# Performance work log

Measured on AMD Instinct MI355X. Metric: run time of the kernel, lower is better.

## Reference

```python
import jax, jax.numpy as jnp
import numpy as np

MODEL_DIM = 128
N_FRAMES = 128
N_SAMPLES = 32768
N_TABLES = 8
TABLE_SIZE = 512
BATCH = 8
N_FREQS = 16


def _mlp(x, w1, b1, w2, b2, w3, b3):
    # LinearOutputStack(channels, 3, ...): Linear -> lrelu -> Linear -> lrelu -> Linear
    h = jax.nn.leaky_relu(x @ w1 + b1, 0.2)
    h = jax.nn.leaky_relu(h @ w2 + b2, 0.2)
    return h @ w3 + b3


def _pos_encoded(t, n_freqs=N_FREQS):
    # (t, 1 + 2*n_freqs) = (t, 33): raw position plus sin/cos at geometric freqs
    pos = jnp.linspace(-1.0, 1.0, t, dtype=jnp.float32)
    scales = (2.0 ** jnp.arange(n_freqs, dtype=jnp.float32)) * jnp.pi
    ang = pos[:, None] * scales[None, :]
    return jnp.concatenate([pos[:, None], jnp.sin(ang), jnp.cos(ang)], axis=-1)


def _interp_linear(env, out_size):
    # torch F.interpolate(mode='linear', align_corners=False) from (B, F) to (B, out_size)
    f = env.shape[-1]
    coord = (jnp.arange(out_size, dtype=jnp.float32) + 0.5) * (f / out_size) - 0.5
    i0 = jnp.floor(coord)
    frac = (coord - i0).astype(env.dtype)
    i0c = jnp.clip(i0, 0, f - 1).astype(jnp.int32)
    i1c = jnp.clip(i0 + 1, 0, f - 1).astype(jnp.int32)
    return env[:, i0c] * (1.0 - frac) + env[:, i1c] * frac


def setup_inputs() -> dict:
    key = jax.random.key(0)
    ks = jax.random.split(key, 16)
    wi = 0.02  # weight_init from Experiment
    d = MODEL_DIM

    def lin(k, i, o):
        return jax.random.normal(k, (i, o), jnp.float32) * wi

    inp = {
        "x": jax.random.normal(ks[0], (BATCH, d), jnp.float32),
        "wavetables": jax.random.uniform(ks[1], (N_TABLES, TABLE_SIZE), jnp.float32, -1.0, 1.0),
    }
    specs = {"tc": (d, N_TABLES), "env": (d, N_FRAMES), "pos": (33, d), "sk": (d, TABLE_SIZE)}
    i = 2
    for name, (cin, cout) in specs.items():
        k1, k2, k3 = jax.random.split(ks[i], 3)
        inp[f"{name}_w1"] = lin(k1, cin, d)
        inp[f"{name}_b1"] = jnp.zeros((d,), jnp.float32)
        inp[f"{name}_w2"] = lin(k2, d, d)
        inp[f"{name}_b2"] = jnp.zeros((d,), jnp.float32)
        inp[f"{name}_w3"] = lin(k3, d, cout)
        inp[f"{name}_b3"] = jnp.zeros((cout,), jnp.float32)
        i += 1
    return inp


def reference(x, wavetables,
              tc_w1, tc_b1, tc_w2, tc_b2, tc_w3, tc_b3,
              env_w1, env_b1, env_w2, env_b2, env_w3, env_b3,
              pos_w1, pos_b1, pos_w2, pos_b2, pos_w3, pos_b3,
              sk_w1, sk_b1, sk_w2, sk_b2, sk_w3, sk_b3):
    # table choice: softmax then hard max (straight value * gathered table)
    c = jax.nn.softmax(_mlp(x, tc_w1, tc_b1, tc_w2, tc_b2, tc_w3, tc_b3), axis=-1)
    values = jnp.max(c, axis=-1)          # (B,)
    indices = jnp.argmax(c, axis=-1)      # (B,)

    mx = jnp.max(wavetables, axis=-1, keepdims=True)
    wt = wavetables / (mx + 1e-8)
    sel = wt[indices]                     # (B, TABLE_SIZE)

    env = jnp.abs(_mlp(x, env_w1, env_b1, env_w2, env_b2, env_w3, env_b3))  # (B, N_FRAMES)
    env = _interp_linear(env, N_SAMPLES)  # (B, N_SAMPLES)

    # pos encoding is identical across batch; embed once then broadcast (same math)
    pe = _pos_encoded(N_SAMPLES)          # (T, 33)
    pos = _mlp(pe, pos_w1, pos_b1, pos_w2, pos_b2, pos_w3, pos_b3)  # (T, D)
    pos = pos[None, :, :] + x[:, None, :]  # (B, T, D)

    sk = jax.nn.softmax(_mlp(pos, sk_w1, sk_b1, sk_w2, sk_b2, sk_w3, sk_b3), axis=-1)  # (B, T, K)

    # selected_tables (B,1,K) @ kernel^T (B,K,T) -> (B,1,T)
    sampled = jnp.einsum('bk,btk->bt', sel, sk)
    sampled = sampled * env * values[:, None]
    return sampled[:, None, :]
```

## Files before the change

### kernel.cpp

```cpp
#include <hip/hip_runtime.h>
#include <math.h>

#define D 128
#define B 8
#define T_SAMP 32768
#define K 512
#define NT 8
#define NFRM 128

#define WS_C1   0
#define WS_ENV8 1024
#define WS_SEL  2048
#define WS_VAL  6144
#define WS_B3P  6160
#define WSBF_BYTE 32768
#define OP1 0
#define OP2 9216
#define OP3 26624
#define OS1 44032
#define OS2 61440
#define OS3 78848
#define WTOT 148480
#define WS_NEED (WSBF_BYTE + WTOT*2)

typedef __attribute__((ext_vector_type(8))) short short8;
typedef __attribute__((ext_vector_type(4))) float f32x4;

#define LOG2E 1.4426950408889634f

__device__ __forceinline__ float lrelu(float v){ return fmaxf(v, 0.2f*v); }

__device__ __forceinline__ unsigned cvtpk(float lo, float hi){
    unsigned r;
    asm("v_cvt_pk_bf16_f32 %0, %1, %2" : "=v"(r) : "v"(lo), "v"(hi));
    return r;
}
__device__ __forceinline__ unsigned short bfr(float f){
    unsigned u = __builtin_bit_cast(unsigned, f); u += 0x7fffu + ((u>>16)&1u);
    return (unsigned short)(u>>16);
}
__device__ __forceinline__ float bf2f(short s){
    unsigned u = ((unsigned)(unsigned short)s) << 16;
    return __builtin_bit_cast(float, u);
}
__device__ __forceinline__ float exp2fast(float x){
#if __has_builtin(__builtin_amdgcn_exp2f)
    return __builtin_amdgcn_exp2f(x);
#else
    return __expf(x*0.6931471805599453f);
#endif
}
__device__ __forceinline__ float sin_rev(float fr){
#if __has_builtin(__builtin_amdgcn_sinf)
    return __builtin_amdgcn_sinf(fr);
#else
    return __sinf(fr*6.283185307179586f);
#endif
}
__device__ __forceinline__ float cos_rev(float fr){
#if __has_builtin(__builtin_amdgcn_cosf)
    return __builtin_amdgcn_cosf(fr);
#else
    return __cosf(fr*6.283185307179586f);
#endif
}
__device__ __forceinline__ float pe_val(float pf, int j){
    if (j == 0) return pf;
    if (j > 32) return 0.f;
    const bool is_sin = (j <= 16);
    int e = is_sin ? (j + 125) : (j + 109);
    float sc = __builtin_bit_cast(float, ((unsigned)e) << 23);
    float u = pf * sc;
    float fr = u - floorf(u);
    return is_sin ? sin_rev(fr) : cos_rev(fr);
}

#define VMCNT0 asm volatile("s_waitcnt vmcnt(0)" ::: "memory")

__device__ void layer128(const float* __restrict__ in, const float* __restrict__ w,
                         const float* __restrict__ bias, float* __restrict__ outp,
                         int tid, int mode)
{
    int n = tid & 127, bg = tid >> 7;
    const float* i0 = in + (bg*4+0)*D;
    const float* i1 = in + (bg*4+1)*D;
    const float* i2 = in + (bg*4+2)*D;
    const float* i3 = in + (bg*4+3)*D;
    float bb = bias[n];
    float a0=bb,a1=bb,a2=bb,a3=bb;
    for (int j=0;j<D;j++){
        float wv = w[j*D+n];
        a0 = fmaf(i0[j], wv, a0);
        a1 = fmaf(i1[j], wv, a1);
        a2 = fmaf(i2[j], wv, a2);
        a3 = fmaf(i3[j], wv, a3);
    }
    if (mode==0){ a0=lrelu(a0);a1=lrelu(a1);a2=lrelu(a2);a3=lrelu(a3); }
    else if (mode==1){ a0=fabsf(a0);a1=fabsf(a1);a2=fabsf(a2);a3=fabsf(a3); }
    outp[(bg*4+0)*D+n]=a0;
    outp[(bg*4+1)*D+n]=a1;
    outp[(bg*4+2)*D+n]=a2;
    outp[(bg*4+3)*D+n]=a3;
}

__global__ __launch_bounds__(256) void setup_kernel(
    const float* __restrict__ x, const float* __restrict__ wt,
    const float* __restrict__ tc_w1, const float* __restrict__ tc_b1,
    const float* __restrict__ tc_w2, const float* __restrict__ tc_b2,
    const float* __restrict__ tc_w3, const float* __restrict__ tc_b3,
    const float* __restrict__ env_w1, const float* __restrict__ env_b1,
    const float* __restrict__ env_w2, const float* __restrict__ env_b2,
    const float* __restrict__ env_w3, const float* __restrict__ env_b3,
    const float* __restrict__ sk_w1, const float* __restrict__ sk_b1,
    const float* __restrict__ pos_w1, const float* __restrict__ pos_w2,
    const float* __restrict__ pos_w3, const float* __restrict__ sk_w2,
    const float* __restrict__ sk_w3, const float* __restrict__ sk_b3,
    float* __restrict__ ws)
{
    __shared__ float xl[B*D], buf1[B*D], buf2[B*D];
    __shared__ float lgts[B*NT], pmax[NT*8], mxr[NT];
    __shared__ int idxl[B];
    int tid = threadIdx.x;

    if (blockIdx.x != 0){
        int idx = (blockIdx.x - 1)*256 + tid;
        if (idx >= WTOT) return;
        unsigned short* wb = (unsigned short*)((char*)ws + WSBF_BYTE);
        float v;
        if (idx < OP2){
            int n = idx/72, k = idx%72;
            v = (k < 33) ? pos_w1[k*D + n] : 0.f;
        } else if (idx < OS3){
            int r = idx - OP2; int wsel = r/17408; int i = r%17408;
            int n = i/136, k = i%136;
            const float* W = wsel==0?pos_w2: wsel==1?pos_w3: wsel==2? sk_w1 : sk_w2;
            v = (k < 128) ? W[k*D + n] : 0.f;
        } else {
            int i = idx - OS3; int n = i/136, k = i%136;
            v = (k < 128) ? sk_w3[k*K + n] : 0.f;
        }
        wb[idx] = bfr(v);
        return;
    }

    for (int i=tid;i<B*D;i+=256) xl[i]=x[i];
    for (int i=tid;i<K;i+=256) ws[WS_B3P+i] = sk_b3[i]*LOG2E;
    __syncthreads();
    layer128(xl, tc_w1, tc_b1, buf1, tid, 0);
    __syncthreads();
    layer128(buf1, tc_w2, tc_b2, buf2, tid, 0);
    __syncthreads();
    if (tid < 64){
        int b = tid>>3, n = tid&7;
        float a = tc_b3[n];
        for (int j=0;j<D;j++) a = fmaf(buf2[b*D+j], tc_w3[j*NT+n], a);
        lgts[b*NT+n] = a;
    } else if (tid < 128){
        int r = (tid-64)>>3, p = tid&7;
        float m = -1e30f;
        for (int k=p*64;k<p*64+64;k++) m = fmaxf(m, wt[r*K+k]);
        pmax[r*8+p] = m;
    }
    __syncthreads();
    if (tid < 8){
        int b = tid; float m = -1e30f; int idx = 0;
        for (int n=0;n<NT;n++){ float v = lgts[b*NT+n]; if (v > m){ m=v; idx=n; } }
        float S = 0.f;
        for (int n=0;n<NT;n++) S += expf(lgts[b*NT+n]-m);
        ws[WS_VAL+b] = 1.0f/S;
        idxl[b] = idx;
    } else if (tid < 16){
        int r = tid-8; float m = -1e30f;
        for (int p=0;p<8;p++) m = fmaxf(m, pmax[r*8+p]);
        mxr[r] = m;
    }
    __syncthreads();
    for (int o=tid;o<B*K;o+=256){
        int b = o>>9, k = o&(K-1);
        int id = idxl[b];
        ws[WS_SEL+o] = wt[id*K+k] / (mxr[id] + 1e-8f);
    }
    layer128(xl, env_w1, env_b1, buf1, tid, 0);
    __syncthreads();
    layer128(buf1, env_w2, env_b2, buf2, tid, 0);
    __syncthreads();
    layer128(buf2, env_w3, env_b3, ws+WS_ENV8, tid, 1);
    layer128(xl, sk_w1, sk_b1, ws+WS_C1, tid, 2);
}

template<int NKT, int KSTR, bool ACT>
__device__ __forceinline__ void layerF(const short8* aw,
                                       const unsigned char* inb, unsigned char* outb,
                                       const float* biasp, int wv, int lg, int lc)
{
    const f32x4 z = {0.f,0.f,0.f,0.f};
    f32x4 bb = z;
    if (biasp) bb = *(const f32x4*)(biasp + 16*wv + 4*lg);
    #pragma unroll
    for (int rt=0;rt<2;rt++){
        f32x4 d = z;
        #pragma unroll
        for (int kt=0;kt<NKT;kt++){
            short8 bf = *(const short8*)(inb + ((16*rt+lc)*KSTR + 32*kt + 8*lg)*2);
            d = __builtin_amdgcn_mfma_f32_16x16x32_bf16(aw[kt], bf, d, 0,0,0);
        }
        float o0 = d[0]+bb[0], o1 = d[1]+bb[1], o2 = d[2]+bb[2], o3 = d[3]+bb[3];
        if (ACT){ o0=lrelu(o0); o1=lrelu(o1); o2=lrelu(o2); o3=lrelu(o3); }
        uint2 u; u.x = cvtpk(o0,o1); u.y = cvtpk(o2,o3);
        *(uint2*)(outb + ((16*rt+lc)*136 + 16*wv + 4*lg)*2) = u;
    }
}

__global__ __launch_bounds__(512, 4) void synth6(
    const float* __restrict__ pos_b1, const float* __restrict__ pos_b2,
    const float* __restrict__ pos_b3, const float* __restrict__ sk_b2,
    const float* __restrict__ ws, float* __restrict__ out)
{
    __shared__ __align__(16) unsigned char lds[34816];
    unsigned char* abA = lds;
    unsigned char* abB = lds + 9216;
    unsigned char* PEb = abB;

    const int tid = threadIdx.x;
    const int wv = tid >> 6, lane = tid & 63, lg = lane >> 4, lc = lane & 15;
    const int t0 = blockIdx.x * 32;
    const unsigned short* wg16 = (const unsigned short*)((const char*)ws + WSBF_BYTE);
    const f32x4 z = {0.f,0.f,0.f,0.f};

    short8 aw1[2];
    #pragma unroll
    for (int kt=0;kt<2;kt++)
        aw1[kt] = *(const short8*)(wg16 + OP1 + (16*wv+lc)*72 + 32*kt + 8*lg);
    for (int i = tid; i < 1152; i += 512){
        int r = i/36, j0 = (i - r*36)*2;
        float pf = (float)(-1.0 + 2.0*(double)(t0+r)/32767.0);
        float v0 = pe_val(pf, j0);
        float v1 = pe_val(pf, j0+1);
        *(unsigned*)(PEb + (r*72 + j0)*2) = cvtpk(v0, v1);
    }
    __syncthreads();

    short8 awn[4];
    #pragma unroll
    for (int kt=0;kt<4;kt++)
        awn[kt] = *(const short8*)(wg16 + OP2 + (16*wv+lc)*136 + 32*kt + 8*lg);
    layerF<2,72,true>(aw1, PEb, abA, pos_b1, wv, lg, lc);
    __syncthreads();

    {
        short8 awp[4];
        #pragma unroll
        for (int kt=0;kt<4;kt++)
            awp[kt] = *(const short8*)(wg16 + OP3 + (16*wv+lc)*136 + 32*kt + 8*lg);
        layerF<4,136,true>(awn, abA, abB, pos_b2, wv, lg, lc);
        #pragma unroll
        for (int kt=0;kt<4;kt++) awn[kt] = awp[kt];
    }
    __syncthreads();

    {
        short8 awp[4];
        #pragma unroll
        for (int kt=0;kt<4;kt++)
            awp[kt] = *(const short8*)(wg16 + OS1 + (16*wv+lc)*136 + 32*kt + 8*lg);
        layerF<4,136,false>(awn, abB, abA, pos_b3, wv, lg, lc);
        #pragma unroll
        for (int kt=0;kt<4;kt++) awn[kt] = awp[kt];
    }
    __syncthreads();

    layerF<4,136,false>(awn, abA, abB, nullptr, wv, lg, lc);
    __syncthreads();

    {
        const unsigned char* src = (const unsigned char*)(wg16 + OS2);
        for (int c = wv; c < 34; c += 8)
            if (c < 9 || c >= 18)
                __builtin_amdgcn_global_load_lds(
                    (const __attribute__((address_space(1))) unsigned int*)(src + (c<<10) + lane*16),
                    (__attribute__((address_space(3))) unsigned int*)(lds + (c<<10)), 16, 0, 0);
    }

    short8 hf[2][4];
    {
        const int b = lc & 7;
        const float* c1g = ws + WS_C1 + b*128;
        #pragma unroll
        for (int rtl=0;rtl<2;rtl++){
            int tl = 4*wv + 2*rtl + (lc>>3);
            #pragma unroll
            for (int kt=0;kt<4;kt++){
                short8 a1v = *(const short8*)(abB + (tl*136 + 32*kt + 8*lg)*2);
                const float* cp = c1g + 32*kt + 8*lg;
                f32x4 c0 = *(const f32x4*)cp;
                f32x4 c1v = *(const f32x4*)(cp+4);
                float h[8];
                #pragma unroll
                for (int e=0;e<4;e++){
                    h[e]   = lrelu(bf2f(a1v[e])   + c0[e]);
                    h[4+e] = lrelu(bf2f(a1v[4+e]) + c1v[e]);
                }
                uint4 t4; t4.x=cvtpk(h[0],h[1]); t4.y=cvtpk(h[2],h[3]);
                t4.z=cvtpk(h[4],h[5]); t4.w=cvtpk(h[6],h[7]);
                hf[rtl][kt] = __builtin_bit_cast(short8, t4);
            }
        }
    }
    __syncthreads();

    {
        const unsigned char* src = (const unsigned char*)(wg16 + OS2);
        for (int c = 9 + wv; c < 18; c += 8)
            __builtin_amdgcn_global_load_lds(
                (const __attribute__((address_space(1))) unsigned int*)(src + (c<<10) + lane*16),
                (__attribute__((address_space(3))) unsigned int*)(lds + (c<<10)), 16, 0, 0);
    }
    VMCNT0; __syncthreads();

    short8 h2B[2][4];
    {
        const int sA = (2*(lg&1))*16 + lc;
        const int sB = sA + 16;
        const bool hi = (lg>>1) != 0;
        __builtin_amdgcn_s_setprio(1);
        #pragma unroll
        for (int kt2=0; kt2<4; kt2++){
            unsigned dpk[2][2][2];
            #pragma unroll
            for (int p=0;p<2;p++){
                int n2t = 2*kt2+p;
                short8 aw[4];
                #pragma unroll
                for (int kt=0;kt<4;kt++)
                    aw[kt] = *(const short8*)(lds + ((16*n2t+lc)*136 + 32*kt + 8*lg)*2);
                f32x4 b2 = *(const f32x4*)(sk_b2 + 16*n2t + 4*lg);
                #pragma unroll
                for (int rtl=0;rtl<2;rtl++){
                    f32x4 d = z;
                    #pragma unroll
                    for (int kt=0;kt<4;kt++)
                        d = __builtin_amdgcn_mfma_f32_16x16x32_bf16(aw[kt], hf[rtl][kt], d, 0,0,0);
                    float o0=lrelu(d[0]+b2[0]), o1=lrelu(d[1]+b2[1]);
                    float o2=lrelu(d[2]+b2[2]), o3=lrelu(d[3]+b2[3]);
                    dpk[p][rtl][0] = cvtpk(o0,o1);
                    dpk[p][rtl][1] = cvtpk(o2,o3);
                }
            }
            #pragma unroll
            for (int rtl=0;rtl<2;rtl++){
                unsigned a0 = (unsigned)__shfl((int)dpk[0][rtl][0], sA, 64);
                unsigned b0 = (unsigned)__shfl((int)dpk[1][rtl][0], sA, 64);
                unsigned a1 = (unsigned)__shfl((int)dpk[0][rtl][1], sA, 64);
                unsigned b1 = (unsigned)__shfl((int)dpk[1][rtl][1], sA, 64);
                unsigned a2 = (unsigned)__shfl((int)dpk[0][rtl][0], sB, 64);
                unsigned b2u= (unsigned)__shfl((int)dpk[1][rtl][0], sB, 64);
                unsigned a3 = (unsigned)__shfl((int)dpk[0][rtl][1], sB, 64);
                unsigned b3u= (unsigned)__shfl((int)dpk[1][rtl][1], sB, 64);
                uint4 uu;
                uu.x = hi ? b0 : a0;  uu.y = hi ? b1 : a1;
                uu.z = hi ? b2u : a2; uu.w = hi ? b3u : a3;
                h2B[rtl][kt2] = __builtin_bit_cast(short8, uu);
            }
        }
        __builtin_amdgcn_s_setprio(0);
    }
    __syncthreads();

    float SSa[2][4], WWa[2][4];
    #pragma unroll
    for (int r=0;r<2;r++)
        #pragma unroll
        for (int q=0;q<4;q++){ SSa[r][q]=0.f; WWa[r][q]=0.f; }

    auto stage = [&](int elemoff, unsigned char* dst, int nchunks){
        const unsigned char* src = (const unsigned char*)(wg16 + elemoff);
        for (int c = wv; c < nchunks; c += 8)
            __builtin_amdgcn_global_load_lds(
                (const __attribute__((address_space(1))) unsigned int*)(src + (c<<10) + lane*16),
                (__attribute__((address_space(3))) unsigned int*)(dst + (c<<10)), 16, 0, 0);
    };

    stage(OS3, lds, 17); VMCNT0; __syncthreads();
    const float* selg = ws + WS_SEL + (lc & 7)*512;
    const float* b3g  = ws + WS_B3P;
    for (int c=0;c<8;c++){
        const unsigned char* slot = lds + (c&1)*17408;
        if (c < 7) stage(OS3 + (c+1)*8704, lds + ((c+1)&1)*17408, 17);
        __builtin_amdgcn_s_setprio(1);
        #pragma unroll
        for (int nl=0;nl<4;nl++){
            int n3t = 4*c + nl;
            short8 bw[4];
            #pragma unroll
            for (int kt=0;kt<4;kt++)
                bw[kt] = *(const short8*)(slot + ((16*nl+lc)*136 + 32*kt + 8*lg)*2);
            f32x4 d3[2]; d3[0]=z; d3[1]=z;
            #pragma unroll
            for (int rtl=0;rtl<2;rtl++){
                #pragma unroll
                for (int kt=0;kt<4;kt++)
                    d3[rtl] = __builtin_amdgcn_mfma_f32_16x16x32_bf16(bw[kt], h2B[rtl][kt], d3[rtl], 0,0,0);
            }
            f32x4 b3 = *(const f32x4*)(b3g + 16*n3t + 4*lg);
            f32x4 sv = *(const f32x4*)(selg + 16*n3t + 4*lg);
            #pragma unroll
            for (int rtl=0;rtl<2;rtl++){
                #pragma unroll
                for (int q=0;q<4;q++){
                    float e = exp2fast(fmaf(d3[rtl][q], LOG2E, b3[q]));
                    SSa[rtl][q] += e;
                    WWa[rtl][q] = fmaf(e, sv[q], WWa[rtl][q]);
                }
            }
        }
        __builtin_amdgcn_s_setprio(0);
        VMCNT0; __syncthreads();
    }

    #pragma unroll
    for (int rtl=0;rtl<2;rtl++){
        float s = SSa[rtl][0]+SSa[rtl][1]+SSa[rtl][2]+SSa[rtl][3];
        float w = WWa[rtl][0]+WWa[rtl][1]+WWa[rtl][2]+WWa[rtl][3];
        s += __shfl_xor(s, 16, 64); s += __shfl_xor(s, 32, 64);
        w += __shfl_xor(w, 16, 64); w += __shfl_xor(w, 32, 64);
        if (lg == 0){
            int tl = 4*wv + 2*rtl + (lc>>3);
            int b  = lc & 7;
            int t  = t0 + tl;
            float coord = (t + 0.5f)*(1.0f/256.0f) - 0.5f;
            float fi = floorf(coord); float frac = coord - fi;
            int i0 = (int)fi; int i1 = i0 + 1;
            i0 = min(max(i0,0),NFRM-1); i1 = min(max(i1,0),NFRM-1);
            float e0 = ws[WS_ENV8 + b*NFRM + i0], e1 = ws[WS_ENV8 + b*NFRM + i1];
            float envv = e0*(1.0f-frac) + e1*frac;
            out[b*T_SAMP + t] = (w/s) * envv * ws[WS_VAL+b];
        }
    }
}

extern "C" void kernel_launch(void* const* d_in, const int* in_sizes, int n_in,
                              void* d_out, int out_size, void* d_ws, size_t ws_size,
                              hipStream_t stream)
{
    (void)in_sizes; (void)n_in; (void)out_size;
    const float* x       = (const float*)d_in[0];
    const float* wt      = (const float*)d_in[1];
    const float* tc_w1   = (const float*)d_in[2];
    const float* tc_b1   = (const float*)d_in[3];
    const float* tc_w2   = (const float*)d_in[4];
    const float* tc_b2   = (const float*)d_in[5];
    const float* tc_w3   = (const float*)d_in[6];
    const float* tc_b3   = (const float*)d_in[7];
    const float* env_w1  = (const float*)d_in[8];
    const float* env_b1  = (const float*)d_in[9];
    const float* env_w2  = (const float*)d_in[10];
    const float* env_b2  = (const float*)d_in[11];
    const float* env_w3  = (const float*)d_in[12];
    const float* env_b3  = (const float*)d_in[13];
    const float* pos_w1  = (const float*)d_in[14];
    const float* pos_b1  = (const float*)d_in[15];
    const float* pos_w2  = (const float*)d_in[16];
    const float* pos_b2  = (const float*)d_in[17];
    const float* pos_w3  = (const float*)d_in[18];
    const float* pos_b3  = (const float*)d_in[19];
    const float* sk_w1   = (const float*)d_in[20];
    const float* sk_b1   = (const float*)d_in[21];
    const float* sk_w2   = (const float*)d_in[22];
    const float* sk_b2   = (const float*)d_in[23];
    const float* sk_w3   = (const float*)d_in[24];
    const float* sk_b3   = (const float*)d_in[25];
    float* ws  = (float*)d_ws;
    float* out = (float*)d_out;

    if (ws_size < (size_t)WS_NEED) return;

    hipLaunchKernelGGL(setup_kernel, dim3(1 + (WTOT+255)/256), dim3(256), 0, stream,
        x, wt, tc_w1, tc_b1, tc_w2, tc_b2, tc_w3, tc_b3,
        env_w1, env_b1, env_w2, env_b2, env_w3, env_b3,
        sk_w1, sk_b1, pos_w1, pos_w2, pos_w3, sk_w2, sk_w3, sk_b3, ws);

    hipLaunchKernelGGL(synth6, dim3(T_SAMP/32), dim3(512), 0, stream,
        pos_b1, pos_b2, pos_b3, sk_b2, ws, out);
}
```

Before: 104.2 us.

## Store weights and activations in MFMA fragment-packed layout, split setup MLP blocks

Weights are pre-packed in the setup kernel into per-fragment 1KB chunks matching the MFMA lane order, so weight and activation loads in the synth kernel become contiguous lane*16 reads without row padding. Activation buffers in LDS use the same fragment layout, which shrinks LDS and staging chunk counts. The setup kernel moves the env and sk first-layer MLPs to a second block so they run in parallel with the table-choice path. The softmax accumulators are also reduced to scalars per row. The risk is possible LDS bank conflicts from the new layout and more complex index math.

```diff
diff --git a/kernel.cpp b/kernel.cpp
--- a/kernel.cpp
+++ b/kernel.cpp
@@ -14,13 +14,13 @@
 #define WS_VAL  6144
 #define WS_B3P  6160
 #define WSBF_BYTE 32768
-#define OP1 0
-#define OP2 9216
-#define OP3 26624
-#define OS1 44032
-#define OS2 61440
-#define OS3 78848
-#define WTOT 148480
+#define FP1 0
+#define FP2 8192
+#define FP3 24576
+#define FS1 40960
+#define FS2 57344
+#define FS3 73728
+#define WTOT 139264
 #define WS_NEED (WSBF_BYTE + WTOT*2)
 
 typedef __attribute__((ext_vector_type(8))) short short8;
@@ -88,6 +88,7 @@
     const float* i3 = in + (bg*4+3)*D;
     float bb = bias[n];
     float a0=bb,a1=bb,a2=bb,a3=bb;
+    #pragma unroll 4
     for (int j=0;j<D;j++){
         float wv = w[j*D+n];
         a0 = fmaf(i0[j], wv, a0);
@@ -122,30 +123,40 @@
     __shared__ int idxl[B];
     int tid = threadIdx.x;
 
-    if (blockIdx.x != 0){
-        int idx = (blockIdx.x - 1)*256 + tid;
+    if (blockIdx.x >= 2){
+        int idx = (blockIdx.x - 2)*256 + tid;
         if (idx >= WTOT) return;
         unsigned short* wb = (unsigned short*)((char*)ws + WSBF_BYTE);
-        float v;
-        if (idx < OP2){
-            int n = idx/72, k = idx%72;
-            v = (k < 33) ? pos_w1[k*D + n] : 0.f;
-        } else if (idx < OS3){
-            int r = idx - OP2; int wsel = r/17408; int i = r%17408;
-            int n = i/136, k = i%136;
-            const float* W = wsel==0?pos_w2: wsel==1?pos_w3: wsel==2? sk_w1 : sk_w2;
-            v = (k < 128) ? W[k*D + n] : 0.f;
-        } else {
-            int i = idx - OS3; int n = i/136, k = i%136;
-            v = (k < 128) ? sk_w3[k*K + n] : 0.f;
-        }
+        int r; const float* Wp; int ncols = D; int nkt = 4; bool p1 = false;
+        if (idx < FP2){ r = idx - FP1; Wp = pos_w1; nkt = 2; p1 = true; }
+        else if (idx < FP3){ r = idx - FP2; Wp = pos_w2; }
+        else if (idx < FS1){ r = idx - FP3; Wp = pos_w3; }
+        else if (idx < FS2){ r = idx - FS1; Wp = sk_w1; }
+        else if (idx < FS3){ r = idx - FS2; Wp = sk_w2; }
+        else { r = idx - FS3; Wp = sk_w3; ncols = K; }
+        int frag = r >> 9, lane = (r >> 3) & 63, e = r & 7;
+        int nt2 = frag / nkt, kt = frag - nt2*nkt;
+        int k = 32*kt + 8*(lane>>4) + e;
+        int n = 16*nt2 + (lane&15);
+        float v = (p1 && k >= 33) ? 0.f : Wp[k*ncols + n];
         wb[idx] = bfr(v);
         return;
     }
 
     for (int i=tid;i<B*D;i+=256) xl[i]=x[i];
-    for (int i=tid;i<K;i+=256) ws[WS_B3P+i] = sk_b3[i]*LOG2E;
-    __syncthreads();
+    __syncthreads();
+
+    if (blockIdx.x == 1){
+        for (int i=tid;i<K;i+=256) ws[WS_B3P+i] = sk_b3[i]*LOG2E;
+        layer128(xl, env_w1, env_b1, buf1, tid, 0);
+        __syncthreads();
+        layer128(buf1, env_w2, env_b2, buf2, tid, 0);
+        __syncthreads();
+        layer128(buf2, env_w3, env_b3, ws+WS_ENV8, tid, 1);
+        layer128(xl, sk_w1, sk_b1, ws+WS_C1, tid, 2);
+        return;
+    }
+
     layer128(xl, tc_w1, tc_b1, buf1, tid, 0);
     __syncthreads();
     layer128(buf1, tc_w2, tc_b2, buf2, tid, 0);
@@ -153,6 +164,7 @@
     if (tid < 64){
         int b = tid>>3, n = tid&7;
         float a = tc_b3[n];
+        #pragma unroll 4
         for (int j=0;j<D;j++) a = fmaf(buf2[b*D+j], tc_w3[j*NT+n], a);
         lgts[b*NT+n] = a;
     } else if (tid < 128){
@@ -180,107 +192,104 @@
         int id = idxl[b];
         ws[WS_SEL+o] = wt[id*K+k] / (mxr[id] + 1e-8f);
     }
-    layer128(xl, env_w1, env_b1, buf1, tid, 0);
-    __syncthreads();
-    layer128(buf1, env_w2, env_b2, buf2, tid, 0);
-    __syncthreads();
-    layer128(buf2, env_w3, env_b3, ws+WS_ENV8, tid, 1);
-    layer128(xl, sk_w1, sk_b1, ws+WS_C1, tid, 2);
-}
-
-template<int NKT, int KSTR, bool ACT>
+}
+
+template<int NKT_IN, bool ACT>
 __device__ __forceinline__ void layerF(const short8* aw,
                                        const unsigned char* inb, unsigned char* outb,
                                        const float* biasp, int wv, int lg, int lc)
 {
     const f32x4 z = {0.f,0.f,0.f,0.f};
+    const int lane16 = (lg*16 + lc)*16;
+    const int obase = ((wv>>1)<<10) + (((2*(wv&1) + (lg>>1))*16 + lc)<<4) + ((lg&1)<<3);
     f32x4 bb = z;
     if (biasp) bb = *(const f32x4*)(biasp + 16*wv + 4*lg);
     #pragma unroll
     for (int rt=0;rt<2;rt++){
         f32x4 d = z;
         #pragma unroll
-        for (int kt=0;kt<NKT;kt++){
-            short8 bf = *(const short8*)(inb + ((16*rt+lc)*KSTR + 32*kt + 8*lg)*2);
+        for (int kt=0;kt<NKT_IN;kt++){
+            short8 bf = *(const short8*)(inb + ((rt*NKT_IN+kt)<<10) + lane16);
             d = __builtin_amdgcn_mfma_f32_16x16x32_bf16(aw[kt], bf, d, 0,0,0);
         }
         float o0 = d[0]+bb[0], o1 = d[1]+bb[1], o2 = d[2]+bb[2], o3 = d[3]+bb[3];
         if (ACT){ o0=lrelu(o0); o1=lrelu(o1); o2=lrelu(o2); o3=lrelu(o3); }
         uint2 u; u.x = cvtpk(o0,o1); u.y = cvtpk(o2,o3);
-        *(uint2*)(outb + ((16*rt+lc)*136 + 16*wv + 4*lg)*2) = u;
-    }
-}
-
-__global__ __launch_bounds__(512, 4) void synth6(
+        *(uint2*)(outb + (rt<<12) + obase) = u;
+    }
+}
+
+__global__ __launch_bounds__(512, 4) void synth7(
     const float* __restrict__ pos_b1, const float* __restrict__ pos_b2,
     const float* __restrict__ pos_b3, const float* __restrict__ sk_b2,
     const float* __restrict__ ws, float* __restrict__ out)
 {
-    __shared__ __align__(16) unsigned char lds[34816];
+    __shared__ __align__(16) unsigned char lds[32768];
     unsigned char* abA = lds;
-    unsigned char* abB = lds + 9216;
+    unsigned char* abB = lds + 8192;
     unsigned char* PEb = abB;
 
     const int tid = threadIdx.x;
     const int wv = tid >> 6, lane = tid & 63, lg = lane >> 4, lc = lane & 15;
+    const int lane16 = lane*16;
     const int t0 = blockIdx.x * 32;
     const unsigned short* wg16 = (const unsigned short*)((const char*)ws + WSBF_BYTE);
     const f32x4 z = {0.f,0.f,0.f,0.f};
 
+    auto stage = [&](int elemoff, unsigned char* dst, int nchunks){
+        const unsigned char* src = (const unsigned char*)(wg16 + elemoff);
+        for (int c = wv; c < nchunks; c += 8)
+            __builtin_amdgcn_global_load_lds(
+                (const __attribute__((address_space(1))) unsigned int*)(src + (c<<10) + lane16),
+                (__attribute__((address_space(3))) unsigned int*)(dst + (c<<10)), 16, 0, 0);
+    };
+
     short8 aw1[2];
     #pragma unroll
     for (int kt=0;kt<2;kt++)
-        aw1[kt] = *(const short8*)(wg16 + OP1 + (16*wv+lc)*72 + 32*kt + 8*lg);
-    for (int i = tid; i < 1152; i += 512){
-        int r = i/36, j0 = (i - r*36)*2;
+        aw1[kt] = *(const short8*)(wg16 + FP1 + ((wv*2+kt)<<9) + lane*8);
+    for (int i = tid; i < 1024; i += 512){
+        int r = i >> 5, p = i & 31;
+        int j0 = 2*p;
         float pf = (float)(-1.0 + 2.0*(double)(t0+r)/32767.0);
         float v0 = pe_val(pf, j0);
         float v1 = pe_val(pf, j0+1);
-        *(unsigned*)(PEb + (r*72 + j0)*2) = cvtpk(v0, v1);
+        int kt = j0 >> 5, rem = j0 & 31;
+        int by = (((r>>4)*2 + kt)<<10) + (((rem>>3)*16 + (r&15))<<4) + (rem&7)*2;
+        *(unsigned*)(PEb + by) = cvtpk(v0, v1);
     }
     __syncthreads();
 
     short8 awn[4];
     #pragma unroll
     for (int kt=0;kt<4;kt++)
-        awn[kt] = *(const short8*)(wg16 + OP2 + (16*wv+lc)*136 + 32*kt + 8*lg);
-    layerF<2,72,true>(aw1, PEb, abA, pos_b1, wv, lg, lc);
-    __syncthreads();
-
+        awn[kt] = *(const short8*)(wg16 + FP2 + ((wv*4+kt)<<9) + lane*8);
+    layerF<2,true>(aw1, PEb, abA, pos_b1, wv, lg, lc);
+    __syncthreads();
     {
         short8 awp[4];
         #pragma unroll
         for (int kt=0;kt<4;kt++)
-            awp[kt] = *(const short8*)(wg16 + OP3 + (16*wv+lc)*136 + 32*kt + 8*lg);
-        layerF<4,136,true>(awn, abA, abB, pos_b2, wv, lg, lc);
+            awp[kt] = *(const short8*)(wg16 + FP3 + ((wv*4+kt)<<9) + lane*8);
+        layerF<4,true>(awn, abA, abB, pos_b2, wv, lg, lc);
         #pragma unroll
         for (int kt=0;kt<4;kt++) awn[kt] = awp[kt];
     }
     __syncthreads();
-
     {
         short8 awp[4];
         #pragma unroll
         for (int kt=0;kt<4;kt++)
-            awp[kt] = *(const short8*)(wg16 + OS1 + (16*wv+lc)*136 + 32*kt + 8*lg);
-        layerF<4,136,false>(awn, abB, abA, pos_b3, wv, lg, lc);
+            awp[kt] = *(const short8*)(wg16 + FS1 + ((wv*4+kt)<<9) + lane*8);
+        layerF<4,false>(awn, abB, abA, pos_b3, wv, lg, lc);
         #pragma unroll
         for (int kt=0;kt<4;kt++) awn[kt] = awp[kt];
     }
     __syncthreads();
-
-    layerF<4,136,false>(awn, abA, abB, nullptr, wv, lg, lc);
-    __syncthreads();
-
-    {
-        const unsigned char* src = (const unsigned char*)(wg16 + OS2);
-        for (int c = wv; c < 34; c += 8)
-            if (c < 9 || c >= 18)
-                __builtin_amdgcn_global_load_lds(
-                    (const __attribute__((address_space(1))) unsigned int*)(src + (c<<10) + lane*16),
-                    (__attribute__((address_space(3))) unsigned int*)(lds + (c<<10)), 16, 0, 0);
-    }
-
+    layerF<4,false>(awn, abA, abB, nullptr, wv, lg, lc);
+    __syncthreads();
+
+    stage(FS2, lds, 8);
     short8 hf[2][4];
     {
         const int b = lc & 7;
@@ -288,9 +297,10 @@
         #pragma unroll
         for (int rtl=0;rtl<2;rtl++){
             int tl = 4*wv + 2*rtl + (lc>>3);
+            int fr = tl >> 4, lrow = tl & 15;
             #pragma unroll
             for (int kt=0;kt<4;kt++){
-                short8 a1v = *(const short8*)(abB + (tl*136 + 32*kt + 8*lg)*2);
+                short8 a1v = *(const short8*)(abB + ((fr*4+kt)<<10) + ((lg*16+lrow)<<4));
                 const float* cp = c1g + 32*kt + 8*lg;
                 f32x4 c0 = *(const f32x4*)cp;
                 f32x4 c1v = *(const f32x4*)(cp+4);
@@ -309,10 +319,10 @@
     __syncthreads();
 
     {
-        const unsigned char* src = (const unsigned char*)(wg16 + OS2);
-        for (int c = 9 + wv; c < 18; c += 8)
+        const unsigned char* src = (const unsigned char*)(wg16 + FS2);
+        for (int c = 8 + wv; c < 32; c += 8)
             __builtin_amdgcn_global_load_lds(
-                (const __attribute__((address_space(1))) unsigned int*)(src + (c<<10) + lane*16),
+                (const __attribute__((address_space(1))) unsigned int*)(src + (c<<10) + lane16),
                 (__attribute__((address_space(3))) unsigned int*)(lds + (c<<10)), 16, 0, 0);
     }
     VMCNT0; __syncthreads();
@@ -332,7 +342,7 @@
                 short8 aw[4];
                 #pragma unroll
                 for (int kt=0;kt<4;kt++)
-                    aw[kt] = *(const short8*)(lds + ((16*n2t+lc)*136 + 32*kt + 8*lg)*2);
+                    aw[kt] = *(const short8*)(lds + ((n2t*4+kt)<<10) + lane16);
                 f32x4 b2 = *(const f32x4*)(sk_b2 + 16*n2t + 4*lg);
                 #pragma unroll
                 for (int rtl=0;rtl<2;rtl++){
@@ -366,26 +376,15 @@
     }
     __syncthreads();
 
-    float SSa[2][4], WWa[2][4];
-    #pragma unroll
-    for (int r=0;r<2;r++)
-        #pragma unroll
-        for (int q=0;q<4;q++){ SSa[r][q]=0.f; WWa[r][q]=0.f; }
-
-    auto stage = [&](int elemoff, unsigned char* dst, int nchunks){
-        const unsigned char* src = (const unsigned char*)(wg16 + elemoff);
-        for (int c = wv; c < nchunks; c += 8)
-            __builtin_amdgcn_global_load_lds(
-                (const __attribute__((address_space(1))) unsigned int*)(src + (c<<10) + lane*16),
-                (__attribute__((address_space(3))) unsigned int*)(dst + (c<<10)), 16, 0, 0);
-    };
-
-    stage(OS3, lds, 17); VMCNT0; __syncthreads();
+    float SSa[2], WWa[2];
+    SSa[0]=0.f; SSa[1]=0.f; WWa[0]=0.f; WWa[1]=0.f;
+
+    stage(FS3, lds, 16); VMCNT0; __syncthreads();
     const float* selg = ws + WS_SEL + (lc & 7)*512;
     const float* b3g  = ws + WS_B3P;
     for (int c=0;c<8;c++){
-        const unsigned char* slot = lds + (c&1)*17408;
-        if (c < 7) stage(OS3 + (c+1)*8704, lds + ((c+1)&1)*17408, 17);
+        const unsigned char* slot = lds + (c&1)*16384;
+        if (c < 7) stage(FS3 + (c+1)*8192, lds + ((c+1)&1)*16384, 16);
         __builtin_amdgcn_s_setprio(1);
         #pragma unroll
         for (int nl=0;nl<4;nl++){
@@ -393,7 +392,7 @@
             short8 bw[4];
             #pragma unroll
             for (int kt=0;kt<4;kt++)
-                bw[kt] = *(const short8*)(slot + ((16*nl+lc)*136 + 32*kt + 8*lg)*2);
+                bw[kt] = *(const short8*)(slot + ((nl*4+kt)<<10) + lane16);
             f32x4 d3[2]; d3[0]=z; d3[1]=z;
             #pragma unroll
             for (int rtl=0;rtl<2;rtl++){
@@ -405,12 +404,13 @@
             f32x4 sv = *(const f32x4*)(selg + 16*n3t + 4*lg);
             #pragma unroll
             for (int rtl=0;rtl<2;rtl++){
-                #pragma unroll
-                for (int q=0;q<4;q++){
-                    float e = exp2fast(fmaf(d3[rtl][q], LOG2E, b3[q]));
-                    SSa[rtl][q] += e;
-                    WWa[rtl][q] = fmaf(e, sv[q], WWa[rtl][q]);
-                }
+                float e0 = exp2fast(fmaf(d3[rtl][0], LOG2E, b3[0]));
+                float e1 = exp2fast(fmaf(d3[rtl][1], LOG2E, b3[1]));
+                float e2 = exp2fast(fmaf(d3[rtl][2], LOG2E, b3[2]));
+                float e3 = exp2fast(fmaf(d3[rtl][3], LOG2E, b3[3]));
+                SSa[rtl] += (e0+e1) + (e2+e3);
+                float w = fmaf(e0, sv[0], fmaf(e1, sv[1], fmaf(e2, sv[2], e3*sv[3])));
+                WWa[rtl] += w;
             }
         }
         __builtin_amdgcn_s_setprio(0);
@@ -419,8 +419,8 @@
 
     #pragma unroll
     for (int rtl=0;rtl<2;rtl++){
-        float s = SSa[rtl][0]+SSa[rtl][1]+SSa[rtl][2]+SSa[rtl][3];
-        float w = WWa[rtl][0]+WWa[rtl][1]+WWa[rtl][2]+WWa[rtl][3];
+        float s = SSa[rtl];
+        float w = WWa[rtl];
         s += __shfl_xor(s, 16, 64); s += __shfl_xor(s, 32, 64);
         w += __shfl_xor(w, 16, 64); w += __shfl_xor(w, 32, 64);
         if (lg == 0){
@@ -474,11 +474,11 @@
 
     if (ws_size < (size_t)WS_NEED) return;
 
-    hipLaunchKernelGGL(setup_kernel, dim3(1 + (WTOT+255)/256), dim3(256), 0, stream,
+    hipLaunchKernelGGL(setup_kernel, dim3(2 + (WTOT+255)/256), dim3(256), 0, stream,
         x, wt, tc_w1, tc_b1, tc_w2, tc_b2, tc_w3, tc_b3,
         env_w1, env_b1, env_w2, env_b2, env_w3, env_b3,
         sk_w1, sk_b1, pos_w1, pos_w2, pos_w3, sk_w2, sk_w3, sk_b3, ws);
 
-    hipLaunchKernelGGL(synth6, dim3(T_SAMP/32), dim3(512), 0, stream,
+    hipLaunchKernelGGL(synth7, dim3(T_SAMP/32), dim3(512), 0, stream,
         pos_b1, pos_b2, pos_b3, sk_b2, ws, out);
 }
```

After: 92.03 us. 1.13x faster.
